# Performance work log

Hardware: AMD Instinct MI355X
Metric: run time of the kernel (lower is better)

The kernel has to match this reference:

```python
import jax, jax.numpy as jnp
import numpy as np

N = 33           # n_nodes (fixed by lstm1 input_size = 512*33)
T = 1024         # seq_length
E_RAND = 64      # random directed edges
E = E_RAND + N   # plus self-loops (PyG GATv2Conv add_self_loops=True)
H1, C1 = 8, 64   # gat1: heads, out_channels
C2 = 512         # gat2: out_channels, 1 head
D_IN, D_EDGE = 2, 3
HID1, HID2, N_CLASSES = 128, 64, 4


def _p(k, shape):
    return jax.random.normal(k, shape, dtype=jnp.float32) * 0.05


def setup_inputs() -> dict:
    key = jax.random.key(0)
    ks = jax.random.split(key, 30)
    src = jax.random.randint(ks[0], (E_RAND,), 0, N)
    dst = jax.random.randint(ks[1], (E_RAND,), 0, N)
    loop = jnp.arange(N)
    edge_index = jnp.stack([jnp.concatenate([src, loop]),
                            jnp.concatenate([dst, loop])]).astype(jnp.int32)
    return {
        'x': jax.random.normal(ks[2], (T, N, D_IN), dtype=jnp.float32),
        'edge_index': edge_index,
        'edge_attr': jax.random.normal(ks[3], (E, D_EDGE), dtype=jnp.float32),
        'g1_wl': _p(ks[4], (D_IN, H1 * C1)),
        'g1_wr': _p(ks[5], (D_IN, H1 * C1)),
        'g1_we': _p(ks[6], (D_EDGE, H1 * C1)),
        'g1_att': _p(ks[7], (H1, C1)),
        'g1_b': _p(ks[8], (H1 * C1,)),
        'g2_wl': _p(ks[9], (H1 * C1, C2)),
        'g2_wr': _p(ks[10], (H1 * C1, C2)),
        'g2_we': _p(ks[11], (D_EDGE, C2)),
        'g2_att': _p(ks[12], (1, C2)),
        'g2_b': _p(ks[13], (C2,)),
        'l1_wih': _p(ks[14], (4 * HID1, N * C2)),
        'l1_whh': _p(ks[15], (4 * HID1, HID1)),
        'l1_bih': _p(ks[16], (4 * HID1,)),
        'l1_bhh': _p(ks[17], (4 * HID1,)),
        'l2_wih': _p(ks[18], (4 * HID2, HID1)),
        'l2_whh': _p(ks[19], (4 * HID2, HID2)),
        'l2_bih': _p(ks[20], (4 * HID2,)),
        'l2_bhh': _p(ks[21], (4 * HID2,)),
        'fc_w': _p(ks[22], (N_CLASSES, HID2)),
        'fc_b': _p(ks[23], (N_CLASSES,)),
    }


def _gatv2(x, src, dst, edge_attr, wl, wr, we, att, bias, heads, ch):
    # GATv2 with edge features, vectorized over the time axis.
    # x: [T,N,Din] -> out [T,N,heads*ch]
    Tt, Nn, _ = x.shape
    xl = (x @ wl).reshape(Tt, Nn, heads, ch)   # source projection
    xr = (x @ wr).reshape(Tt, Nn, heads, ch)   # target projection
    ep = (edge_attr @ we).reshape(-1, heads, ch)
    msg = xl[:, src]                                        # [T,E,H,C]
    e = jax.nn.leaky_relu(msg + xr[:, dst] + ep[None], 0.2)  # GATv2 score input
    logits = jnp.einsum('tehc,hc->eth', e, att)             # edge-first [E,T,H]
    m = jax.ops.segment_max(logits, dst, num_segments=Nn)
    m = jnp.where(jnp.isneginf(m), 0.0, m)
    ex = jnp.exp(logits - m[dst])
    denom = jax.ops.segment_sum(ex, dst, num_segments=Nn)
    alpha = ex / (denom[dst] + 1e-16)                       # [E,T,H]
    out = jax.ops.segment_sum(alpha[..., None] * jnp.swapaxes(msg, 0, 1),
                              dst, num_segments=Nn)          # [N,T,H,C]
    return jnp.swapaxes(out, 0, 1).reshape(Tt, Nn, heads * ch) + bias


def _lstm(xs, wih, whh, bih, bhh):
    # PyTorch LSTM, batch=1, gate order i,f,g,o. xs: [T,D] -> [T,H]
    hd = whh.shape[1]
    def step(carry, xt):
        h, c = carry
        z = xt @ wih.T + h @ whh.T + bih + bhh
        i, f, g, o = jnp.split(z, 4)
        c = jax.nn.sigmoid(f) * c + jax.nn.sigmoid(i) * jnp.tanh(g)
        h = jax.nn.sigmoid(o) * jnp.tanh(c)
        return (h, c), h
    h0 = jnp.zeros((hd,), xs.dtype)
    _, hs = jax.lax.scan(step, (h0, h0), xs)
    return hs


def _forward(edge_index, x, edge_attr, g1_wl, g1_wr, g1_we, g1_att, g1_b,
             g2_wl, g2_wr, g2_we, g2_att, g2_b,
             l1_wih, l1_whh, l1_bih, l1_bhh,
             l2_wih, l2_whh, l2_bih, l2_bhh, fc_w, fc_b):
    src, dst = edge_index[0], edge_index[1]
    h = jax.nn.elu(_gatv2(x, src, dst, edge_attr, g1_wl, g1_wr, g1_we, g1_att, g1_b, H1, C1))
    h = jax.nn.elu(_gatv2(h, src, dst, edge_attr, g2_wl, g2_wr, g2_we, g2_att, g2_b, 1, C2))
    # torch: stack [T,N,512] -> permute(1,0,2) -> reshape(1, T, N*512)
    seq = jnp.transpose(h, (1, 0, 2)).reshape(T, N * C2)
    hs = _lstm(seq, l1_wih, l1_whh, l1_bih, l1_bhh)
    hs = _lstm(hs, l2_wih, l2_whh, l2_bih, l2_bhh)
    return (hs[-1] @ fc_w.T + fc_b)[None, :]  # [1, n_classes]


def reference(x, edge_index, edge_attr, g1_wl, g1_wr, g1_we, g1_att, g1_b,
              g2_wl, g2_wr, g2_we, g2_att, g2_b,
              l1_wih, l1_whh, l1_bih, l1_bhh,
              l2_wih, l2_whh, l2_bih, l2_bhh, fc_w, fc_b):
    return _forward(edge_index, x, edge_attr, g1_wl, g1_wr, g1_we, g1_att, g1_b,
                    g2_wl, g2_wr, g2_we, g2_att, g2_b,
                    l1_wih, l1_whh, l1_bih, l1_bhh,
                    l2_wih, l2_whh, l2_bih, l2_bhh, fc_w, fc_b)
```

## Files before the change

kernel.cpp:

```cpp
#include <hip/hip_runtime.h>

typedef unsigned short u16;
typedef unsigned int   u32;
typedef __attribute__((ext_vector_type(8))) short  short8;
typedef __attribute__((ext_vector_type(8))) unsigned short ushort8;
typedef __attribute__((ext_vector_type(4))) float  f32x4;

#define NT 1024
#define NN 33
#define NE 97

__device__ __forceinline__ float b2f(u16 u){ return __uint_as_float(((u32)u)<<16); }
__device__ __forceinline__ u16 f2b(float f){
    u32 x = __float_as_uint(f);
    return (u16)((x + 0x7fffu + ((x>>16)&1u)) >> 16);
}
__device__ __forceinline__ float sigm(float x){ return 1.f/(1.f+__expf(-x)); }
__device__ __forceinline__ float tanh_(float x){ float e=__expf(2.f*x); return 1.f - 2.f/(e+1.f); }

struct ConvArgs { const void* src[22]; int n[22]; int off[22]; };
__global__ void convert_kernel(ConvArgs a, const u32* raw, int* flag, u16* blob){
    __shared__ int s_isf32;
    if (threadIdx.x==0){
        int hits=0;
        for (int k=0;k<256;k++){
            u32 w = raw[k];
            u32 e = (w>>7)&0xffu;
            if (e>=96u && e<=126u) hits++;
        }
        s_isf32 = (hits>=160) ? 0 : 1;
        if (blockIdx.x==0) *flag = s_isf32;
    }
    __syncthreads();
    bool isf32 = s_isf32!=0;
    int stride = gridDim.x*blockDim.x;
    for (int s=0;s<22;s++){
        int n=a.n[s]; const void* sp=a.src[s]; u16* dp=blob+a.off[s];
        for (int i=blockIdx.x*blockDim.x+threadIdx.x; i<n; i+=stride)
            dp[i] = isf32 ? f2b(((const float*)sp)[i]) : ((const u16*)sp)[i];
    }
}

#define CX      0
#define CEA     67584
#define CG1WL   67880
#define CG1WR   68904
#define CG1WE   69928
#define CG1ATT  71464
#define CG1B    71976
#define CG2WL   72488
#define CG2WR   334632
#define CG2WE   596776
#define CG2ATT  598312
#define CG2B    598824
#define CL1WIH  599336
#define CL1WHH  9250088
#define CL1BIH  9315624
#define CL1BHH  9316136
#define CL2WIH  9316648
#define CL2WHH  9349416
#define CL2BIH  9365800
#define CL2BHH  9366056
#define CFCW    9366312
#define CFCB    9366568

__global__ void prep_kernel(const int* ei, const u16* ea,
                            const u16* g1_we, const u16* g2_we,
                            const u16* g2_wl, const u16* g2_wr,
                            const u16* w1hh, const u16* w2ih, const u16* w2hh,
                            int* csr, float* ep1, float* ep2, u16* wlrt,
                            u16* w1p, u16* w2ip, u16* w2hp)
{
    int b = blockIdx.x, tid = threadIdx.x;
    if (b==0){
        if (tid == 0) {
            int cnt[NN]; for (int n=0;n<NN;n++) cnt[n]=0;
            for (int e=0;e<NE;e++) cnt[ei[NE+e]]++;
            int off=0;
            for (int n=0;n<NN;n++){ csr[n]=off; off+=cnt[n]; }
            csr[NN]=off;
            int pos[NN]; for (int n=0;n<NN;n++) pos[n]=csr[n];
            for (int e=0;e<NE;e++){ int d=ei[NE+e]; csr[34+pos[d]]=e; pos[d]++; }
            for (int e=0;e<NE;e++){ csr[131+e]=ei[e]; csr[228+e]=ei[NE+e]; }
        }
        for (int i=tid; i<NE*512; i+=256) {
            int e = i>>9, hc = i&511;
            float a0=b2f(ea[e*3]), a1=b2f(ea[e*3+1]), a2=b2f(ea[e*3+2]);
            ep1[i] = a0*b2f(g1_we[hc]) + a1*b2f(g1_we[512+hc]) + a2*b2f(g1_we[1024+hc]);
            ep2[i] = a0*b2f(g2_we[hc]) + a1*b2f(g2_we[512+hc]) + a2*b2f(g2_we[1024+hc]);
        }
    } else if (b<=1024){
        int i = (b-1)*256 + tid;
        int k = i>>9, c = i&511;
        wlrt[c*512 + k]        = g2_wl[i];
        wlrt[(c+512)*512 + k]  = g2_wr[i];
    } else {
        int i0 = (b-1025)*256 + tid;
        int stride = 64*256;
        for (int j=i0; j<65536; j+=stride){
            int r=j>>7, k=j&127, u=r>>2, g=r&3;
            w1p[j] = w1hh[(g*128+u)*128 + k];
        }
        for (int j=i0; j<32768; j+=stride){
            int r=j>>7, k=j&127, u=r>>2, g=r&3;
            w2ip[j] = w2ih[(g*64+u)*128 + k];
        }
        for (int j=i0; j<16384; j+=stride){
            int r=j>>6, k=j&63, u=r>>2, g=r&3;
            w2hp[j] = w2hh[(g*64+u)*64 + k];
        }
    }
}

__global__ __launch_bounds__(256) void gat1_kernel(
    const u16* x, const u16* g1_wl, const u16* g1_wr, const u16* g1_att,
    const u16* g1_b, const float* ep1, const int* csr, u16* h1)
{
    __shared__ float wl[2][512], wr[2][512], att[512], bias[512];
    __shared__ float xt[2*NN];
    __shared__ float logits[NE*8];
    __shared__ float mmax[NN*8], den[NN*8];
    __shared__ int s_off[NN+1], s_eid[NE], s_src[NE], s_dst[NE];
    int t = blockIdx.x, tid = threadIdx.x;

    for (int i=tid;i<512;i+=256){
        wl[0][i]=b2f(g1_wl[i]);      wl[1][i]=b2f(g1_wl[512+i]);
        wr[0][i]=b2f(g1_wr[i]);      wr[1][i]=b2f(g1_wr[512+i]);
        att[i]=b2f(g1_att[i]);       bias[i]=b2f(g1_b[i]);
    }
    for (int i=tid;i<2*NN;i+=256) xt[i]=b2f(x[t*(2*NN)+i]);
    if (tid<NN+1) s_off[tid]=csr[tid];
    for (int i=tid;i<NE;i+=256){ s_eid[i]=csr[34+i]; s_src[i]=csr[131+i]; s_dst[i]=csr[228+i]; }
    __syncthreads();

    for (int i=tid; i<NE*8; i+=256) {
        int e=i>>3, h=i&7;
        int s=s_src[e], d=s_dst[e];
        float xs0=xt[s*2], xs1=xt[s*2+1], xd0=xt[d*2], xd1=xt[d*2+1];
        const float* epp = ep1 + e*512 + h*64;
        float acc=0.f;
        #pragma unroll 8
        for (int c=0;c<64;c++){
            int hc=h*64+c;
            float v = xs0*wl[0][hc] + xs1*wl[1][hc]
                    + xd0*wr[0][hc] + xd1*wr[1][hc] + epp[c];
            v = v>0.f ? v : 0.2f*v;
            acc += att[hc]*v;
        }
        logits[i]=acc;
    }
    __syncthreads();
    for (int i=tid; i<NN*8; i+=256) {
        int n=i>>3, h=i&7;
        float m=-1e30f;
        for (int p=s_off[n]; p<s_off[n+1]; ++p){ float v=logits[s_eid[p]*8+h]; m=v>m?v:m; }
        float s=0.f;
        for (int p=s_off[n]; p<s_off[n+1]; ++p) s += __expf(logits[s_eid[p]*8+h]-m);
        mmax[i]=m; den[i]=s+1e-16f;
    }
    __syncthreads();
    for (int i=tid; i<NE*8; i+=256) {
        int h=i&7, d=s_dst[i>>3];
        logits[i] = __expf(logits[i]-mmax[d*8+h]) / den[d*8+h];
    }
    __syncthreads();
    for (int i=tid; i<NN*512; i+=256) {
        int n=i>>9, hc=i&511, h=hc>>6;
        float acc=0.f;
        for (int p=s_off[n]; p<s_off[n+1]; ++p){
            int e=s_eid[p]; int s=s_src[e];
            float xlv = xt[s*2]*wl[0][hc] + xt[s*2+1]*wl[1][hc];
            acc += logits[e*8+h]*xlv;
        }
        acc += bias[hc];
        acc = acc>0.f ? acc : __expf(acc)-1.f;
        h1[(size_t)(t*NN+n)*512 + hc] = f2b(acc);
    }
}

__global__ __launch_bounds__(256) void gemm_nt(
    const u16* __restrict__ A, const u16* __restrict__ B, void* Cout,
    int M, int N, int K, int kChunk, int mode)
{
    __shared__ u16 lds_a[128*32];
    __shared__ u16 lds_b[128*32];
    const int nt = blockIdx.x, mt = blockIdx.y, kc = blockIdx.z;
    const int tid = threadIdx.x;
    const int wave = tid>>6, lane = tid&63;
    const int wm = (wave&1)*64, wn = (wave>>1)*64;
    const int l15 = lane&15, quad = lane>>4;
    const int srow = tid>>2, scol = (tid&3)*8;

    const u16* Ab = A + (size_t)mt*128*K;
    const u16* Bb = B + (size_t)nt*128*K;
    const int k0beg = kc*kChunk, k0end = k0beg + kChunk;

    f32x4 acc[4][4] = {};
    for (int k0 = k0beg; k0 < k0end; k0 += 32) {
        #pragma unroll
        for (int r = 0; r < 2; ++r) {
            int row = srow + r*64;
            const u16* ga = Ab + (size_t)row*K + k0 + scol;
            const u16* gb = Bb + (size_t)row*K + k0 + scol;
            u16* la = &lds_a[(r*64 + wave*16)*32];
            u16* lb = &lds_b[(r*64 + wave*16)*32];
            __builtin_amdgcn_global_load_lds((const u32*)ga, (u32*)la, 16, 0, 0);
            __builtin_amdgcn_global_load_lds((const u32*)gb, (u32*)lb, 16, 0, 0);
        }
        __syncthreads();
        short8 af[4], bfr[4];
        #pragma unroll
        for (int i=0;i<4;i++) af[i]  = *(const short8*)&lds_a[(wm + i*16 + l15)*32 + quad*8];
        #pragma unroll
        for (int j=0;j<4;j++) bfr[j] = *(const short8*)&lds_b[(wn + j*16 + l15)*32 + quad*8];
        #pragma unroll
        for (int i=0;i<4;i++)
            #pragma unroll
            for (int j=0;j<4;j++)
                acc[i][j] = __builtin_amdgcn_mfma_f32_16x16x32_bf16(af[i], bfr[j], acc[i][j], 0,0,0);
        __syncthreads();
    }
    if (mode == 0) {
        u16* Cb = (u16*)Cout;
        #pragma unroll
        for (int i=0;i<4;i++)
            #pragma unroll
            for (int j=0;j<4;j++)
                #pragma unroll
                for (int r=0;r<4;r++){
                    int row = mt*128 + wm + i*16 + quad*4 + r;
                    int col = nt*128 + wn + j*16 + l15;
                    Cb[(size_t)row*N + col] = f2b(acc[i][j][r]);
                }
    } else {
        float* Cb = (float*)Cout + (size_t)kc*M*N;
        #pragma unroll
        for (int i=0;i<4;i++)
            #pragma unroll
            for (int j=0;j<4;j++)
                #pragma unroll
                for (int r=0;r<4;r++){
                    int row = mt*128 + wm + i*16 + quad*4 + r;
                    int col = nt*128 + wn + j*16 + l15;
                    Cb[(size_t)row*N + col] = acc[i][j][r];
                }
    }
}

__global__ void reduce16_kernel(const float* part, const u16* b1ih, const u16* b1bhh, float* out)
{
    int i = blockIdx.x*256 + threadIdx.x;
    float s=0.f;
    #pragma unroll
    for (int k=0;k<16;k++) s += part[(size_t)k*524288 + i];
    int t=i>>9, c=i&511;
    s += b2f(b1ih[c]) + b2f(b1bhh[c]);
    out[t*512 + ((c&127)<<2) + (c>>7)] = s;
}

__global__ __launch_bounds__(256) void gat2_kernel(
    const u16* C, const u16* g2_att, const u16* g2_b, const float* ep2,
    const int* csr, u16* h2)
{
    __shared__ u16 xl[NN*512];
    __shared__ float att[512], bias[512];
    __shared__ float part[NE*8];
    __shared__ float logit[NE], alpha[NE], mm[NN], dd[NN];
    __shared__ int s_off[NN+1], s_eid[NE], s_src[NE], s_dst[NE];
    int t = blockIdx.x, tid = threadIdx.x;

    for (int i=tid;i<512;i+=256){ att[i]=b2f(g2_att[i]); bias[i]=b2f(g2_b[i]); }
    if (tid<NN+1) s_off[tid]=csr[tid];
    for (int i=tid;i<NE;i+=256){ s_eid[i]=csr[34+i]; s_src[i]=csr[131+i]; s_dst[i]=csr[228+i]; }
    for (int i=tid; i<NN*64; i+=256){
        int n=i>>6, q=i&63;
        *(ushort8*)&xl[n*512+q*8] = *(const ushort8*)&C[(size_t)(t*NN+n)*1024 + q*8];
    }
    __syncthreads();

    for (int i=tid; i<NE*8; i+=256){
        int e=i>>3, q=i&7;
        int s=s_src[e], d=s_dst[e];
        const u16* xrp = C + (size_t)(t*NN+d)*1024 + 512 + q*64;
        const float* epp = ep2 + e*512 + q*64;
        const u16* xlp = xl + s*512 + q*64;
        float acc=0.f;
        #pragma unroll 8
        for (int c=0;c<64;c++){
            float v = b2f(xlp[c]) + b2f(xrp[c]) + epp[c];
            v = v>0.f ? v : 0.2f*v;
            acc += att[q*64+c]*v;
        }
        part[i]=acc;
    }
    __syncthreads();
    for (int i=tid;i<NE;i+=256){
        float s=0.f;
        #pragma unroll
        for (int q=0;q<8;q++) s+=part[i*8+q];
        logit[i]=s;
    }
    __syncthreads();
    for (int i=tid;i<NN;i+=256){
        float m=-1e30f;
        for (int p=s_off[i];p<s_off[i+1];++p){ float v=logit[s_eid[p]]; m=v>m?v:m; }
        float s=0.f;
        for (int p=s_off[i];p<s_off[i+1];++p) s+=__expf(logit[s_eid[p]]-m);
        mm[i]=m; dd[i]=s+1e-16f;
    }
    __syncthreads();
    for (int i=tid;i<NE;i+=256) alpha[i]=__expf(logit[i]-mm[s_dst[i]])/dd[s_dst[i]];
    __syncthreads();
    for (int i=tid;i<NN*512;i+=256){
        int n=i>>9, c=i&511;
        float acc=0.f;
        for (int p=s_off[n];p<s_off[n+1];++p){ int e=s_eid[p]; acc += alpha[e]*b2f(xl[s_src[e]*512+c]); }
        acc += bias[c];
        acc = acc>0.f ? acc : __expf(acc)-1.f;
        h2[(size_t)n*524288 + (size_t)t*512 + c] = f2b(acc);
    }
}

__global__ __launch_bounds__(512) void lstm_fused_kernel(
    const float* __restrict__ pre1p,
    const u16* __restrict__ w1p,
    const u16* __restrict__ w2ip, const u16* __restrict__ w2hp,
    const u16* b2ih, const u16* b2bhh,
    const u16* fc_w, const u16* fc_b, const int* flag,
    u32* ring, u32* flags, void* outv)
{
    const int tid = threadIdx.x;
    const int wave = tid>>6, lane = tid&63;
    const int l15 = lane&15, quad = lane>>4;
    const f32x4 fz = {0.f,0.f,0.f,0.f};

    if (blockIdx.x == 0) {
        __shared__ __align__(16) u16 hb1[2][128];
        __shared__ __align__(16) u16 hchunk[16*128];
        u32* hc32 = (u32*)hchunk;

        short8 af1[4][4];
        #pragma unroll
        for (int i=0;i<4;i++)
            #pragma unroll
            for (int c=0;c<4;c++)
                af1[i][c] = *(const short8*)&w1p[(size_t)(wave*64 + i*16 + l15)*128 + c*32 + quad*8];

        const int uu = wave*16 + ((l15<4)?l15:0)*4 + quad;
        const bool gatelane = (l15<4);
        float cst = 0.f;
        if (tid<128) hb1[0][tid]=0;

        const u16* hqA = &hb1[0][quad*8];
        const u16* hqB = &hb1[1][quad*8];

        float4 pf_cur = {0.f,0.f,0.f,0.f};
        if (gatelane) pf_cur = *(const float4*)&pre1p[uu*4];

        for (int k=0;k<=1024;k++){
            if (k>=16 && (k&15)==0){
                int c = (k>>4) - 1;
                u32* dst = ring + c*1024;
                __hip_atomic_store(&dst[tid],     hc32[tid],     __ATOMIC_RELAXED, __HIP_MEMORY_SCOPE_AGENT);
                __hip_atomic_store(&dst[tid+512], hc32[tid+512], __ATOMIC_RELAXED, __HIP_MEMORY_SCOPE_AGENT);
                __syncthreads();
                if (tid==0)
                    __hip_atomic_store(&flags[c], (u32)(c+1), __ATOMIC_RELEASE, __HIP_MEMORY_SCOPE_AGENT);
            }
            if (k<1024){
                float4 pf_next = {0.f,0.f,0.f,0.f};
                if (gatelane && k<1023)
                    pf_next = *(const float4*)&pre1p[(size_t)(k+1)*512 + uu*4];
                const u16* hq = (k&1) ? hqB : hqA;
                short8 b0 = *(const short8*)&hq[0];
                short8 b1 = *(const short8*)&hq[32];
                short8 b2 = *(const short8*)&hq[64];
                short8 b3 = *(const short8*)&hq[96];
                f32x4 acc[4];
                #pragma unroll
                for (int i=0;i<4;i++){
                    f32x4 a = __builtin_amdgcn_mfma_f32_16x16x32_bf16(af1[i][0], b0, fz, 0,0,0);
                    a = __builtin_amdgcn_mfma_f32_16x16x32_bf16(af1[i][1], b1, a, 0,0,0);
                    a = __builtin_amdgcn_mfma_f32_16x16x32_bf16(af1[i][2], b2, a, 0,0,0);
                    a = __builtin_amdgcn_mfma_f32_16x16x32_bf16(af1[i][3], b3, a, 0,0,0);
                    acc[i] = a;
                }
                f32x4 z = acc[0];
                z = (l15==1) ? acc[1] : z;
                z = (l15==2) ? acc[2] : z;
                z = (l15==3) ? acc[3] : z;
                if (gatelane){
                    float zi = z[0]+pf_cur.x;
                    float zf = z[1]+pf_cur.y;
                    float zg = z[2]+pf_cur.z;
                    float zo = z[3]+pf_cur.w;
                    cst = sigm(zf)*cst + sigm(zi)*tanh_(zg);
                    float ho = sigm(zo)*tanh_(cst);
                    u16 hv = f2b(ho);
                    hb1[(k+1)&1][uu] = hv;
                    hchunk[(k&15)*128 + uu] = hv;
                }
                pf_cur = pf_next;
            }
            __syncthreads();
        }
    } else {
        __shared__ __align__(16) u16 h1c[16*136];
        __shared__ __align__(16) float z2l[16*264];
        __shared__ __align__(16) u16 hb2[2][64];
        __shared__ float hf[64];

        short8 af2[2][2];
        #pragma unroll
        for (int j=0;j<2;j++)
            #pragma unroll
            for (int c=0;c<2;c++)
                af2[j][c] = *(const short8*)&w2hp[(size_t)(wave*32 + j*16 + l15)*64 + c*32 + quad*8];
        short8 af3[2][4];
        #pragma unroll
        for (int j=0;j<2;j++)
            #pragma unroll
            for (int c=0;c<4;c++)
                af3[j][c] = *(const short8*)&w2ip[(size_t)(wave*32 + j*16 + l15)*128 + c*32 + quad*8];

        int u2 = 0; float bz0=0,bz1=0,bz2=0,bz3=0;
        if (l15<2){
            u2 = wave*8 + l15*4 + quad;
            bz0 = b2f(b2ih[u2])     + b2f(b2bhh[u2]);
            bz1 = b2f(b2ih[64+u2])  + b2f(b2bhh[64+u2]);
            bz2 = b2f(b2ih[128+u2]) + b2f(b2bhh[128+u2]);
            bz3 = b2f(b2ih[192+u2]) + b2f(b2bhh[192+u2]);
        }
        float cst = 0.f;
        if (tid<64) hb2[1][tid]=0;
        __syncthreads();

        u32* h1c32 = (u32*)h1c;
        for (int c=0;c<64;c++){
            if (tid==0){
                while (__hip_atomic_load(&flags[c], __ATOMIC_ACQUIRE, __HIP_MEMORY_SCOPE_AGENT) != (u32)(c+1))
                    __builtin_amdgcn_s_sleep(2);
            }
            __syncthreads();
            const u32* src = ring + c*1024;
            #pragma unroll
            for (int j=0;j<2;j++){
                int i = tid + j*512;
                u32 v = __hip_atomic_load(&src[i], __ATOMIC_RELAXED, __HIP_MEMORY_SCOPE_AGENT);
                int s = i>>6, w2 = i&63;
                h1c32[s*68 + w2] = v;
            }
            __syncthreads();
            short8 hbv[4];
            #pragma unroll
            for (int cc=0;cc<4;cc++)
                hbv[cc] = *(const short8*)&h1c[l15*136 + cc*32 + quad*8];
            f32x4 ba[2] = {fz,fz};
            #pragma unroll
            for (int cc=0;cc<4;cc++){
                ba[0] = __builtin_amdgcn_mfma_f32_16x16x32_bf16(af3[0][cc], hbv[cc], ba[0], 0,0,0);
                ba[1] = __builtin_amdgcn_mfma_f32_16x16x32_bf16(af3[1][cc], hbv[cc], ba[1], 0,0,0);
            }
            *(f32x4*)&z2l[l15*264 + (wave*8 + quad)*4]     = ba[0];
            *(f32x4*)&z2l[l15*264 + (wave*8 + 4 + quad)*4] = ba[1];
            __syncthreads();
            for (int s=0;s<16;s++){
                int sg = c*16 + s;
                const u16* hp2 = hb2[(sg+1)&1];
                short8 g0 = *(const short8*)&hp2[quad*8];
                short8 g1 = *(const short8*)&hp2[32+quad*8];
                f32x4 a0 = __builtin_amdgcn_mfma_f32_16x16x32_bf16(af2[0][0], g0, fz, 0,0,0);
                a0 = __builtin_amdgcn_mfma_f32_16x16x32_bf16(af2[0][1], g1, a0, 0,0,0);
                f32x4 a1 = __builtin_amdgcn_mfma_f32_16x16x32_bf16(af2[1][0], g0, fz, 0,0,0);
                a1 = __builtin_amdgcn_mfma_f32_16x16x32_bf16(af2[1][1], g1, a1, 0,0,0);
                f32x4 z = (l15==1) ? a1 : a0;
                if (l15<2){
                    const float4 pf = *(const float4*)&z2l[s*264 + u2*4];
                    float zi = z[0]+pf.x+bz0;
                    float zf = z[1]+pf.y+bz1;
                    float zg = z[2]+pf.z+bz2;
                    float zo = z[3]+pf.w+bz3;
                    cst = sigm(zf)*cst + sigm(zi)*tanh_(zg);
                    float ho = sigm(zo)*tanh_(cst);
                    hb2[sg&1][u2] = f2b(ho);
                    hf[u2] = ho;
                }
                __syncthreads();
            }
        }
        if (tid<4){
            float acc = b2f(fc_b[tid]);
            #pragma unroll
            for (int j=0;j<64;j++) acc += hf[j]*b2f(fc_w[tid*64+j]);
            if (*flag) ((float*)outv)[tid] = acc;
            else       ((u16*)outv)[tid]  = f2b(acc);
        }
    }
}

extern "C" void kernel_launch(void* const* d_in, const int* in_sizes, int n_in,
                              void* d_out, int out_size, void* d_ws, size_t ws_size,
                              hipStream_t stream) {
    const int* ei = (const int*)d_in[1];
    char* ws = (char*)d_ws;

    const size_t o_blob = 0;
    const size_t o_h    = 18733184;
    const size_t o_C    = o_h    + 34603008;
    const size_t o_wlrt = o_C    + 69206016;
    const size_t o_ep1  = o_wlrt + 1048576;
    const size_t o_ep2  = o_ep1  + 198656;
    const size_t o_csr  = o_ep2  + 198656;
    const size_t o_pre1 = o_csr  + 2048;
    const size_t o_w1p  = o_pre1 + 2097152;
    const size_t o_w2ip = o_w1p  + 131072;
    const size_t o_w2hp = o_w2ip + 65536;
    const size_t o_ring = o_w2hp + 32768;
    const size_t o_flgs = o_ring + 262144;

    u16*   blob  = (u16*)(ws + o_blob);
    u16*   h_buf = (u16*)(ws + o_h);
    u16*   Cbuf  = (u16*)(ws + o_C);
    u16*   wlrt  = (u16*)(ws + o_wlrt);
    float* ep1   = (float*)(ws + o_ep1);
    float* ep2   = (float*)(ws + o_ep2);
    int*   csr   = (int*)(ws + o_csr);
    int*   flag  = csr + 400;
    float* pre1  = (float*)(ws + o_pre1);
    u16*   w1p   = (u16*)(ws + o_w1p);
    u16*   w2ip  = (u16*)(ws + o_w2ip);
    u16*   w2hp  = (u16*)(ws + o_w2hp);
    u32*   ring  = (u32*)(ws + o_ring);
    u32*   flags = (u32*)(ws + o_flgs);
    float* part  = (float*)(ws + o_C);

    ConvArgs ca;
    const int blob_off[22] = {CX,CEA,CG1WL,CG1WR,CG1WE,CG1ATT,CG1B,
                              CG2WL,CG2WR,CG2WE,CG2ATT,CG2B,
                              CL1WIH,CL1WHH,CL1BIH,CL1BHH,
                              CL2WIH,CL2WHH,CL2BIH,CL2BHH,CFCW,CFCB};
    const int in_idx[22]   = {0,2,3,4,5,6,7,8,9,10,11,12,13,14,15,16,17,18,19,20,21,22};
    for (int s=0;s<22;s++){
        ca.src[s]=d_in[in_idx[s]]; ca.n[s]=in_sizes[in_idx[s]]; ca.off[s]=blob_off[s];
    }
    convert_kernel<<<2048,256,0,stream>>>(ca, (const u32*)d_in[3], flag, blob);

    prep_kernel<<<1089,256,0,stream>>>(ei, blob+CEA, blob+CG1WE, blob+CG2WE,
                                       blob+CG2WL, blob+CG2WR,
                                       blob+CL1WHH, blob+CL2WIH, blob+CL2WHH,
                                       csr, ep1, ep2, wlrt, w1p, w2ip, w2hp);
    gat1_kernel<<<NT,256,0,stream>>>(blob+CX, blob+CG1WL, blob+CG1WR, blob+CG1ATT,
                                     blob+CG1B, ep1, csr, h_buf);
    gemm_nt<<<dim3(8,264,1),256,0,stream>>>(h_buf, wlrt, Cbuf, 33792, 1024, 512, 512, 0);
    gat2_kernel<<<NT,256,0,stream>>>(Cbuf, blob+CG2ATT, blob+CG2B, ep2, csr, h_buf);
    gemm_nt<<<dim3(4,8,16),256,0,stream>>>(h_buf, blob+CL1WIH, part, 1024, 512, 16896, 1056, 1);
    reduce16_kernel<<<2048,256,0,stream>>>(part, blob+CL1BIH, blob+CL1BHH, pre1);
    lstm_fused_kernel<<<2,512,0,stream>>>(pre1,
        w1p, w2ip, w2hp, blob+CL2BIH, blob+CL2BHH,
        blob+CFCW, blob+CFCB, flag, ring, flags, d_out);
}
```

Measured before the change: 1.366 ms.

## Shrink fused LSTM blocks to two waves with more MFMA tiles per wave

Runs the fused LSTM recurrence with 128-thread blocks instead of 512. Each wave now holds four times as many weight fragments in registers and issues 16 (layer 1) or 8 (layer 2) independent MFMA accumulator chains per step, with every lane doing gate math. The aim is cheaper per-step __syncthreads across fewer waves and interleaved independent MFMAs that hide latency on the serial critical path. The cost is much higher register pressure (64 short8 weight fragments plus 16 accumulators), which could cause spills, and more serial MFMA work per wave.

```diff
diff --git a/kernel.cpp b/kernel.cpp
--- a/kernel.cpp
+++ b/kernel.cpp
@@ -321,7 +321,7 @@
     }
 }
 
-__global__ __launch_bounds__(512) void lstm_fused_kernel(
+__global__ __launch_bounds__(128,1) void lstm_fused_kernel(
     const float* __restrict__ pre1p,
     const u16* __restrict__ w1p,
     const u16* __restrict__ w2ip, const u16* __restrict__ w2hp,
@@ -339,57 +339,58 @@
         __shared__ __align__(16) u16 hchunk[16*128];
         u32* hc32 = (u32*)hchunk;
 
-        short8 af1[4][4];
-        #pragma unroll
-        for (int i=0;i<4;i++)
+        short8 af1[16][4];
+        #pragma unroll
+        for (int i=0;i<16;i++)
             #pragma unroll
             for (int c=0;c<4;c++)
-                af1[i][c] = *(const short8*)&w1p[(size_t)(wave*64 + i*16 + l15)*128 + c*32 + quad*8];
-
-        const int uu = wave*16 + ((l15<4)?l15:0)*4 + quad;
-        const bool gatelane = (l15<4);
+                af1[i][c] = *(const short8*)&w1p[(size_t)(wave*256 + i*16 + l15)*128 + c*32 + quad*8];
+
+        const int uu = wave*64 + l15*4 + quad;
         float cst = 0.f;
-        if (tid<128) hb1[0][tid]=0;
+        hb1[0][tid] = 0;
 
         const u16* hqA = &hb1[0][quad*8];
         const u16* hqB = &hb1[1][quad*8];
 
-        float4 pf_cur = {0.f,0.f,0.f,0.f};
-        if (gatelane) pf_cur = *(const float4*)&pre1p[uu*4];
+        float4 pf_cur = *(const float4*)&pre1p[uu*4];
 
         for (int k=0;k<=1024;k++){
             if (k>=16 && (k&15)==0){
                 int c = (k>>4) - 1;
                 u32* dst = ring + c*1024;
-                __hip_atomic_store(&dst[tid],     hc32[tid],     __ATOMIC_RELAXED, __HIP_MEMORY_SCOPE_AGENT);
-                __hip_atomic_store(&dst[tid+512], hc32[tid+512], __ATOMIC_RELAXED, __HIP_MEMORY_SCOPE_AGENT);
+                #pragma unroll
+                for (int j=0;j<8;j++)
+                    __hip_atomic_store(&dst[tid + j*128], hc32[tid + j*128],
+                                       __ATOMIC_RELAXED, __HIP_MEMORY_SCOPE_AGENT);
                 __syncthreads();
                 if (tid==0)
                     __hip_atomic_store(&flags[c], (u32)(c+1), __ATOMIC_RELEASE, __HIP_MEMORY_SCOPE_AGENT);
             }
             if (k<1024){
                 float4 pf_next = {0.f,0.f,0.f,0.f};
-                if (gatelane && k<1023)
+                if (k<1023)
                     pf_next = *(const float4*)&pre1p[(size_t)(k+1)*512 + uu*4];
                 const u16* hq = (k&1) ? hqB : hqA;
                 short8 b0 = *(const short8*)&hq[0];
                 short8 b1 = *(const short8*)&hq[32];
                 short8 b2 = *(const short8*)&hq[64];
                 short8 b3 = *(const short8*)&hq[96];
-                f32x4 acc[4];
-                #pragma unroll
-                for (int i=0;i<4;i++){
-                    f32x4 a = __builtin_amdgcn_mfma_f32_16x16x32_bf16(af1[i][0], b0, fz, 0,0,0);
-                    a = __builtin_amdgcn_mfma_f32_16x16x32_bf16(af1[i][1], b1, a, 0,0,0);
-                    a = __builtin_amdgcn_mfma_f32_16x16x32_bf16(af1[i][2], b2, a, 0,0,0);
-                    a = __builtin_amdgcn_mfma_f32_16x16x32_bf16(af1[i][3], b3, a, 0,0,0);
-                    acc[i] = a;
-                }
+                f32x4 acc[16];
+                #pragma unroll
+                for (int i=0;i<16;i++) acc[i]=fz;
+                #pragma unroll
+                for (int i=0;i<16;i++) acc[i] = __builtin_amdgcn_mfma_f32_16x16x32_bf16(af1[i][0], b0, acc[i], 0,0,0);
+                #pragma unroll
+                for (int i=0;i<16;i++) acc[i] = __builtin_amdgcn_mfma_f32_16x16x32_bf16(af1[i][1], b1, acc[i], 0,0,0);
+                #pragma unroll
+                for (int i=0;i<16;i++) acc[i] = __builtin_amdgcn_mfma_f32_16x16x32_bf16(af1[i][2], b2, acc[i], 0,0,0);
+                #pragma unroll
+                for (int i=0;i<16;i++) acc[i] = __builtin_amdgcn_mfma_f32_16x16x32_bf16(af1[i][3], b3, acc[i], 0,0,0);
                 f32x4 z = acc[0];
-                z = (l15==1) ? acc[1] : z;
-                z = (l15==2) ? acc[2] : z;
-                z = (l15==3) ? acc[3] : z;
-                if (gatelane){
+                #pragma unroll
+                for (int i=1;i<16;i++) z = (l15==i) ? acc[i] : z;
+                {
                     float zi = z[0]+pf_cur.x;
                     float zf = z[1]+pf_cur.y;
                     float zg = z[2]+pf_cur.z;
@@ -410,22 +411,22 @@
         __shared__ __align__(16) u16 hb2[2][64];
         __shared__ float hf[64];
 
-        short8 af2[2][2];
-        #pragma unroll
-        for (int j=0;j<2;j++)
+        short8 af2[8][2];
+        #pragma unroll
+        for (int j=0;j<8;j++)
             #pragma unroll
             for (int c=0;c<2;c++)
-                af2[j][c] = *(const short8*)&w2hp[(size_t)(wave*32 + j*16 + l15)*64 + c*32 + quad*8];
-        short8 af3[2][4];
-        #pragma unroll
-        for (int j=0;j<2;j++)
+                af2[j][c] = *(const short8*)&w2hp[(size_t)(wave*128 + j*16 + l15)*64 + c*32 + quad*8];
+        short8 af3[8][4];
+        #pragma unroll
+        for (int j=0;j<8;j++)
             #pragma unroll
             for (int c=0;c<4;c++)
-                af3[j][c] = *(const short8*)&w2ip[(size_t)(wave*32 + j*16 + l15)*128 + c*32 + quad*8];
+                af3[j][c] = *(const short8*)&w2ip[(size_t)(wave*128 + j*16 + l15)*128 + c*32 + quad*8];
 
         int u2 = 0; float bz0=0,bz1=0,bz2=0,bz3=0;
-        if (l15<2){
-            u2 = wave*8 + l15*4 + quad;
+        if (l15<8){
+            u2 = wave*32 + l15*4 + quad;
             bz0 = b2f(b2ih[u2])     + b2f(b2bhh[u2]);
             bz1 = b2f(b2ih[64+u2])  + b2f(b2bhh[64+u2]);
             bz2 = b2f(b2ih[128+u2]) + b2f(b2bhh[128+u2]);
@@ -444,8 +445,8 @@
             __syncthreads();
             const u32* src = ring + c*1024;
             #pragma unroll
-            for (int j=0;j<2;j++){
-                int i = tid + j*512;
+            for (int j=0;j<8;j++){
+                int i = tid + j*128;
                 u32 v = __hip_atomic_load(&src[i], __ATOMIC_RELAXED, __HIP_MEMORY_SCOPE_AGENT);
                 int s = i>>6, w2 = i&63;
                 h1c32[s*68 + w2] = v;
@@ -455,26 +456,31 @@
             #pragma unroll
             for (int cc=0;cc<4;cc++)
                 hbv[cc] = *(const short8*)&h1c[l15*136 + cc*32 + quad*8];
-            f32x4 ba[2] = {fz,fz};
-            #pragma unroll
-            for (int cc=0;cc<4;cc++){
-                ba[0] = __builtin_amdgcn_mfma_f32_16x16x32_bf16(af3[0][cc], hbv[cc], ba[0], 0,0,0);
-                ba[1] = __builtin_amdgcn_mfma_f32_16x16x32_bf16(af3[1][cc], hbv[cc], ba[1], 0,0,0);
-            }
-            *(f32x4*)&z2l[l15*264 + (wave*8 + quad)*4]     = ba[0];
-            *(f32x4*)&z2l[l15*264 + (wave*8 + 4 + quad)*4] = ba[1];
+            f32x4 ba[8] = {fz,fz,fz,fz,fz,fz,fz,fz};
+            #pragma unroll
+            for (int cc=0;cc<4;cc++)
+                #pragma unroll
+                for (int j=0;j<8;j++)
+                    ba[j] = __builtin_amdgcn_mfma_f32_16x16x32_bf16(af3[j][cc], hbv[cc], ba[j], 0,0,0);
+            #pragma unroll
+            for (int j=0;j<8;j++)
+                *(f32x4*)&z2l[l15*264 + (wave*32 + j*4 + quad)*4] = ba[j];
             __syncthreads();
             for (int s=0;s<16;s++){
                 int sg = c*16 + s;
                 const u16* hp2 = hb2[(sg+1)&1];
                 short8 g0 = *(const short8*)&hp2[quad*8];
                 short8 g1 = *(const short8*)&hp2[32+quad*8];
-                f32x4 a0 = __builtin_amdgcn_mfma_f32_16x16x32_bf16(af2[0][0], g0, fz, 0,0,0);
-                a0 = __builtin_amdgcn_mfma_f32_16x16x32_bf16(af2[0][1], g1, a0, 0,0,0);
-                f32x4 a1 = __builtin_amdgcn_mfma_f32_16x16x32_bf16(af2[1][0], g0, fz, 0,0,0);
-                a1 = __builtin_amdgcn_mfma_f32_16x16x32_bf16(af2[1][1], g1, a1, 0,0,0);
-                f32x4 z = (l15==1) ? a1 : a0;
-                if (l15<2){
+                f32x4 a[8];
+                #pragma unroll
+                for (int j=0;j<8;j++){
+                    f32x4 t0 = __builtin_amdgcn_mfma_f32_16x16x32_bf16(af2[j][0], g0, fz, 0,0,0);
+                    a[j] = __builtin_amdgcn_mfma_f32_16x16x32_bf16(af2[j][1], g1, t0, 0,0,0);
+                }
+                f32x4 z = a[0];
+                #pragma unroll
+                for (int j=1;j<8;j++) z = (l15==j) ? a[j] : z;
+                if (l15<8){
                     const float4 pf = *(const float4*)&z2l[s*264 + u2*4];
                     float zi = z[0]+pf.x+bz0;
                     float zf = z[1]+pf.y+bz1;
@@ -555,7 +561,7 @@
     gat2_kernel<<<NT,256,0,stream>>>(Cbuf, blob+CG2ATT, blob+CG2B, ep2, csr, h_buf);
     gemm_nt<<<dim3(4,8,16),256,0,stream>>>(h_buf, blob+CL1WIH, part, 1024, 512, 16896, 1056, 1);
     reduce16_kernel<<<2048,256,0,stream>>>(part, blob+CL1BIH, blob+CL1BHH, pre1);
-    lstm_fused_kernel<<<2,512,0,stream>>>(pre1,
+    lstm_fused_kernel<<<2,128,0,stream>>>(pre1,
         w1p, w2ip, w2hp, blob+CL2BIH, blob+CL2BHH,
         blob+CFCW, blob+CFCB, flag, ring, flags, d_out);
 }
```

Result: slower. 1.722 ms (+26.0%).
